# Optimization experiments

Measured on AMD Instinct MI355X. Metric: run time of the kernel, lower is better.

## Reference

```python
import jax, jax.numpy as jnp
import numpy as np

N = 1_000_000
H, W = 480, 640
MIN_DEPTH, MAX_DEPTH = 0.0, 30.0


def setup_inputs() -> dict:
    key = jax.random.key(0)
    k1, k2, k3 = jax.random.split(key, 3)
    scale = jnp.array([W - 1, H - 1], dtype=jnp.float32)
    mkpts0_f = jax.random.uniform(k1, (N, 2), dtype=jnp.float32) * scale
    mkpts1_f = jax.random.uniform(k2, (N, 2), dtype=jnp.float32) * scale
    mconf = jax.random.uniform(k3, (N,), dtype=jnp.float32)
    K = jnp.array([[520.0, 0.0, 320.0],
                   [0.0, 520.0, 240.0],
                   [0.0, 0.0, 1.0]], dtype=jnp.float32)
    K0 = K[None]  # [1,3,3]
    K1 = K[None]
    c, s = float(np.cos(0.1)), float(np.sin(0.1))
    T_0to1 = jnp.array([[c, 0.0, s, 0.2],
                        [0.0, 1.0, 0.0, 0.0],
                        [-s, 0.0, c, 0.05],
                        [0.0, 0.0, 0.0, 1.0]], dtype=jnp.float32)[None]  # [1,4,4]
    image0 = jnp.zeros((1, 1, H, W), dtype=jnp.float32)
    m_bids = jnp.zeros((N,), dtype=jnp.int32)  # single batch element
    return {"T_0to1": T_0to1, "K0": K0, "K1": K1, "mconf": mconf,
            "mkpts0_f": mkpts0_f, "mkpts1_f": mkpts1_f,
            "image0": image0, "m_bids": m_bids}


def _triangulate(T_0to1, K0, K1, mconf, kpts0, kpts1):
    # Projection matrices: P0 = K0 @ [I|0], P1 = K1 @ T[:3,:]
    proj_identity = jnp.eye(3, 4, dtype=K0.dtype)
    P0 = K0[0] @ proj_identity          # [3,4]
    P1 = K1[0] @ T_0to1[0, :3, :]       # [3,4]
    P = jnp.stack([P0, P1], axis=0)     # [V=2,3,4]

    pts = jnp.stack([kpts0, kpts1], axis=1)              # [N,2,2]
    conf = jnp.stack([jnp.ones_like(mconf), mconf], 1)   # [N,2] (self conf = 1)

    # A[n,v] = pts[n,v,:,None] * P[v,2,None,:] - P[v,:2]   -> [N,V,2,4]
    A = pts[..., None] * P[None, :, 2, None, :] - P[None, :, :2, :]
    A = A * conf[:, :, None, None]
    A = A.reshape(A.shape[0], 4, 4)                       # [N,4,4]

    # torch.svd returns V with A = U S V^T; jnp gives Vh = V^T.
    _, _, Vh = jnp.linalg.svd(A)
    v = -Vh[:, 3, :]                                      # [N,4] = -V[:,:,3]
    points_3d = v[:, :3] / v[:, 3:4]                      # homogeneous -> euclidean
    # torch clamps to [-1000,1000] only when infs appear; the final depth value
    # after [0,30] clamp + filter is identical either way, so clip unconditionally.
    points_3d = jnp.clip(points_3d, -1000.0, 1000.0)

    z = jnp.clip(points_3d[:, 2], MIN_DEPTH, MAX_DEPTH)
    filt = (z > MIN_DEPTH) & (z < MAX_DEPTH)
    kp3d_val = z * filt.astype(z.dtype)
    return kp3d_val, points_3d


def reference(T_0to1, K0, K1, mconf, mkpts0_f, mkpts1_f, image0, m_bids):
    h, w = image0.shape[-2], image0.shape[-1]
    kp3d_val, _ = _triangulate(T_0to1, K0, K1, mconf, mkpts0_f, mkpts1_f)
    # generate_sparse_depth: depth[0, y, x] = kp3d_val (long() truncation)
    xi = mkpts0_f[:, 0].astype(jnp.int32)
    yi = mkpts0_f[:, 1].astype(jnp.int32)
    depth0_sparse = jnp.zeros((1, h, w), dtype=kp3d_val.dtype).at[0, yi, xi].set(kp3d_val)
    return depth0_sparse, kp3d_val
```

## Files before the change

### kernel.cpp

```cpp
#include <hip/hip_runtime.h>
#include <math.h>

#define N_PTS 1000000
#define H_IMG 480
#define W_IMG 640
#define PIX (H_IMG * W_IMG)
#define TPB 256
#define BPTS 1024
#define NBLK ((N_PTS + BPTS - 1) / BPTS)


#define ROT64(p, q)                                                            \
  do {                                                                         \
    double apq = Mv[p][q];                                                     \
    if (apq != 0.0) {                                                          \
      double app = Mv[p][p], aqq = Mv[q][q];                                   \
      double d = aqq - app;                                                    \
      double r = sqrt(fma(d, d, 4.0 * apq * apq));                             \
      double t = (2.0 * apq) / (d + copysign(r, d));                           \
      double c = rsqrt(fma(t, t, 1.0));                                        \
      double s = t * c;                                                        \
      Mv[p][p] = fma(-t, apq, app);                                            \
      Mv[q][q] = fma(t, apq, aqq);                                             \
      Mv[p][q] = 0.0;                                                          \
      Mv[q][p] = 0.0;                                                          \
      _Pragma("unroll") for (int k = 0; k < 4; k++) {                          \
        if (k != p && k != q) {                                                \
          double akp = Mv[k][p], akq = Mv[k][q];                               \
          double nkp = c * akp - s * akq;                                      \
          double nkq = s * akp + c * akq;                                      \
          Mv[k][p] = nkp; Mv[p][k] = nkp;                                      \
          Mv[k][q] = nkq; Mv[q][k] = nkq;                                      \
        }                                                                      \
      }                                                                        \
      { double v2p = Vr2[p], v2q = Vr2[q];                                     \
        Vr2[p] = c * v2p - s * v2q; Vr2[q] = s * v2p + c * v2q; }              \
      { double v3p = Vr3[p], v3q = Vr3[q];                                     \
        Vr3[p] = c * v3p - s * v3q; Vr3[q] = s * v3p + c * v3q; }              \
    }                                                                          \
  } while (0)

__device__ float tri_point_fp64(int n,
                                const float* __restrict__ T,
                                const float* __restrict__ K0,
                                const float* __restrict__ K1,
                                const float* __restrict__ mconf,
                                const float* __restrict__ kp0,
                                const float* __restrict__ kp1) {
  float2 p0 = ((const float2*)kp0)[n];
  float2 p1 = ((const float2*)kp1)[n];
  double conf = (double)mconf[n];
  double x0 = (double)p0.x, y0 = (double)p0.y;
  double x1 = (double)p1.x, y1 = (double)p1.y;

  double P0[3][4];
#pragma unroll
  for (int i = 0; i < 3; i++) {
#pragma unroll
    for (int j = 0; j < 3; j++) P0[i][j] = (double)K0[i * 3 + j];
    P0[i][3] = 0.0;
  }
  double P1[3][4];
#pragma unroll
  for (int i = 0; i < 3; i++) {
#pragma unroll
    for (int j = 0; j < 4; j++) {
      double s = 0.0;
#pragma unroll
      for (int k = 0; k < 3; k++)
        s += (double)K1[i * 3 + k] * (double)T[k * 4 + j];
      P1[i][j] = s;
    }
  }

  double Mv[4][4];
#pragma unroll
  for (int i = 0; i < 4; i++)
#pragma unroll
    for (int j = 0; j < 4; j++) Mv[i][j] = 0.0;

  double a[4];
#pragma unroll
  for (int j = 0; j < 4; j++) a[j] = x0 * P0[2][j] - P0[0][j];
#pragma unroll
  for (int i = 0; i < 4; i++)
#pragma unroll
    for (int j = 0; j < 4; j++) Mv[i][j] = fma(a[i], a[j], Mv[i][j]);
#pragma unroll
  for (int j = 0; j < 4; j++) a[j] = y0 * P0[2][j] - P0[1][j];
#pragma unroll
  for (int i = 0; i < 4; i++)
#pragma unroll
    for (int j = 0; j < 4; j++) Mv[i][j] = fma(a[i], a[j], Mv[i][j]);
#pragma unroll
  for (int j = 0; j < 4; j++) a[j] = conf * (x1 * P1[2][j] - P1[0][j]);
#pragma unroll
  for (int i = 0; i < 4; i++)
#pragma unroll
    for (int j = 0; j < 4; j++) Mv[i][j] = fma(a[i], a[j], Mv[i][j]);
#pragma unroll
  for (int j = 0; j < 4; j++) a[j] = conf * (y1 * P1[2][j] - P1[1][j]);
#pragma unroll
  for (int i = 0; i < 4; i++)
#pragma unroll
    for (int j = 0; j < 4; j++) Mv[i][j] = fma(a[i], a[j], Mv[i][j]);

  double Vr2[4] = {0.0, 0.0, 1.0, 0.0};
  double Vr3[4] = {0.0, 0.0, 0.0, 1.0};

  for (int sweep = 0; sweep < 4; sweep++) {
    ROT64(0, 1); ROT64(0, 2); ROT64(0, 3);
    ROT64(1, 2); ROT64(1, 3); ROT64(2, 3);
  }

  double e0 = Mv[0][0], e1 = Mv[1][1], e2 = Mv[2][2], e3 = Mv[3][3];
  bool b01 = e1 < e0;
  double ea = b01 ? e1 : e0;
  double za = b01 ? Vr2[1] : Vr2[0];
  double wa = b01 ? Vr3[1] : Vr3[0];
  bool b23 = e3 < e2;
  double eb = b23 ? e3 : e2;
  double zb = b23 ? Vr2[3] : Vr2[2];
  double wb = b23 ? Vr3[3] : Vr3[2];
  bool bf = eb < ea;
  double vz = bf ? zb : za;
  double vw = bf ? wb : wa;

  double z = vz / vw;
  z = fmin(fmax(z, 0.0), 30.0);
  bool filt = (z > 0.0) && (z < 30.0);
  return filt ? (float)z : 0.0f;
}

__global__ __launch_bounds__(TPB) void tri_main(
    const float* __restrict__ T,
    const float* __restrict__ K0,
    const float* __restrict__ K1,
    const float* __restrict__ mconf,
    const float* __restrict__ kp0,
    const float* __restrict__ kp1,
    float* __restrict__ out_kp3d,
    unsigned long long* __restrict__ ws_pix)
{
  __shared__ unsigned short s_list[BPTS];
  __shared__ int s_cnt;

  int tid = threadIdx.x;
  int base = blockIdx.x * BPTS;
  if (tid == 0) s_cnt = 0;
  __syncthreads();

  double P0d[3][4], P1d[3][4];
#pragma unroll
  for (int i = 0; i < 3; i++) {
#pragma unroll
    for (int j = 0; j < 3; j++) P0d[i][j] = (double)K0[i * 3 + j];
    P0d[i][3] = 0.0;
  }
#pragma unroll
  for (int i = 0; i < 3; i++) {
#pragma unroll
    for (int j = 0; j < 4; j++) {
      double s = 0.0;
#pragma unroll
      for (int k = 0; k < 3; k++)
        s += (double)K1[i * 3 + k] * (double)T[k * 4 + j];
      P1d[i][j] = s;
    }
  }

#pragma unroll 1
  for (int r = 0; r < BPTS / TPB; r++) {
    int local = r * TPB + tid;
    int n = base + local;
    if (n >= N_PTS) break;

    float2 p0 = ((const float2*)kp0)[n];
    float2 p1 = ((const float2*)kp1)[n];
    float conff = mconf[n];

    double m00, m01, m02, m03, m11, m12, m13, m22, m23, m33;
    m00 = m01 = m02 = m03 = m11 = m12 = m13 = m22 = m23 = m33 = 0.0;
    {
      double x0 = (double)p0.x, y0 = (double)p0.y;
      double x1 = (double)p1.x, y1 = (double)p1.y;
      double cf = (double)conff;
      double a[4];
#pragma unroll
      for (int rr = 0; rr < 4; rr++) {
        if (rr == 0) {
#pragma unroll
          for (int j = 0; j < 4; j++) a[j] = fma(x0, P0d[2][j], -P0d[0][j]);
        } else if (rr == 1) {
#pragma unroll
          for (int j = 0; j < 4; j++) a[j] = fma(y0, P0d[2][j], -P0d[1][j]);
        } else if (rr == 2) {
#pragma unroll
          for (int j = 0; j < 4; j++)
            a[j] = cf * fma(x1, P1d[2][j], -P1d[0][j]);
        } else {
#pragma unroll
          for (int j = 0; j < 4; j++)
            a[j] = cf * fma(y1, P1d[2][j], -P1d[1][j]);
        }
        m00 = fma(a[0], a[0], m00); m01 = fma(a[0], a[1], m01);
        m02 = fma(a[0], a[2], m02); m03 = fma(a[0], a[3], m03);
        m11 = fma(a[1], a[1], m11); m12 = fma(a[1], a[2], m12);
        m13 = fma(a[1], a[3], m13); m22 = fma(a[2], a[2], m22);
        m23 = fma(a[2], a[3], m23); m33 = fma(a[3], a[3], m33);
      }
    }

    double t1 = (m00 + m11) + (m22 + m33);
    double ms0 = fma(m00, m11, -m01 * m01);
    double ms1 = fma(m00, m12, -m02 * m01);
    double ms2 = fma(m00, m13, -m03 * m01);
    double ms3 = fma(m01, m12, -m02 * m11);
    double ms4 = fma(m01, m13, -m03 * m11);
    double mc0 = fma(m02, m13, -m12 * m03);
    double mc1 = fma(m02, m23, -m22 * m03);
    double mc2 = fma(m02, m33, -m23 * m03);
    double mc3 = fma(m12, m23, -m22 * m13);
    double mc4 = fma(m12, m33, -m23 * m13);
    double mc5 = fma(m22, m33, -m23 * m23);
    double A00 = fma(m11, mc5, fma(-m12, mc4, m13 * mc3));
    double A01 = -fma(m01, mc5, fma(-m02, mc4, m03 * mc3));
    double A11 = fma(m00, mc5, fma(-m02, mc2, m03 * mc1));
    double A02 = fma(m01, mc4, fma(-m11, mc2, m13 * mc0));
    double A03 = -fma(m01, mc3, fma(-m11, mc1, m12 * mc0));
    double A22 = fma(m03, ms4, fma(-m13, ms2, m33 * ms0));
    double A33 = fma(m02, ms3, fma(-m12, ms1, m22 * ms0));
    double t3 = (A00 + A11) + (A22 + A33);
    double t4 = fma(m00, A00, fma(m01, A01, fma(m02, A02, m03 * A03)));
    double q02 = fma(m00, m22, -m02 * m02);
    double q03 = fma(m00, m33, -m03 * m03);
    double q12 = fma(m11, m22, -m12 * m12);
    double q13 = fma(m11, m33, -m13 * m13);
    double t2 = ((ms0 + mc5) + (q02 + q03)) + (q12 + q13);

    double mu = t4 / t3;
    double t1_3 = 3.0 * t1, t1_6 = 6.0 * t1, t2_2 = 2.0 * t2;
#pragma unroll
    for (int it = 0; it < 3; it++) {
      double pv = fma(fma(fma(mu - t1, mu, t2), mu, -t3), mu, t4);
      double pd = fma(fma(fma(4.0, mu, -t1_3), mu, t2_2), mu, -t3);
      double pdd = fma(fma(12.0, mu, -t1_6), mu, t2_2);
      double rad = 3.0 * fma(3.0 * pd, pd, -4.0 * pv * pdd);
      double sq = sqrt(fmax(rad, 0.0));
      double den = pd + copysign(sq, pd);
      mu = mu - 4.0 * pv / den;
    }

    double b00 = m00 - mu, b11 = m11 - mu, b22 = m22 - mu, b33 = m33 - mu;
    double s0 = fma(b00, b11, -m01 * m01);
    double s1 = fma(b00, m12, -m02 * m01);
    double s2 = fma(b00, m13, -m03 * m01);
    double s3 = fma(m01, m12, -m02 * b11);
    double s4 = fma(m01, m13, -m03 * b11);
    double c0 = fma(m02, m13, -m12 * m03);
    double c1 = fma(m02, m23, -b22 * m03);
    double c2 = fma(m02, b33, -m23 * m03);
    double c3 = fma(m12, m23, -b22 * m13);
    double c4 = fma(m12, b33, -m23 * m13);
    double c5 = fma(b22, b33, -m23 * m23);

    double a00 = fma(b11, c5, fma(-m12, c4, m13 * c3));
    double a01 = -fma(m01, c5, fma(-m02, c4, m03 * c3));
    double a11 = fma(b00, c5, fma(-m02, c2, m03 * c1));
    double a02 = fma(m01, c4, fma(-b11, c2, m13 * c0));
    double a12 = -fma(b00, c4, fma(-m01, c2, m03 * c0));
    double a22 = fma(m03, s4, fma(-m13, s2, b33 * s0));
    double a03 = -fma(m01, c3, fma(-b11, c1, m12 * c0));
    double a13 = fma(b00, c3, fma(-m01, c1, m02 * c0));
    double a23 = -fma(m03, s3, fma(-m13, s1, m23 * s0));
    double a33 = fma(m02, s3, fma(-m12, s1, b22 * s0));

    double w10 = a00, w11 = a01, w12 = a02, w13 = a03;
    double bd = fabs(a00);
    { double d1 = fabs(a11);
      bool c = d1 > bd;
      w10 = c ? a01 : w10; w11 = c ? a11 : w11;
      w12 = c ? a12 : w12; w13 = c ? a13 : w13; bd = c ? d1 : bd; }
    { double d2 = fabs(a22);
      bool c = d2 > bd;
      w10 = c ? a02 : w10; w11 = c ? a12 : w11;
      w12 = c ? a22 : w12; w13 = c ? a23 : w13; bd = c ? d2 : bd; }
    { double d3 = fabs(a33);
      bool c = d3 > bd;
      w10 = c ? a03 : w10; w11 = c ? a13 : w11;
      w12 = c ? a23 : w12; w13 = c ? a33 : w13; }

    double u0 = fma(a00, w10, fma(a01, w11, fma(a02, w12, a03 * w13)));
    double u1 = fma(a01, w10, fma(a11, w11, fma(a12, w12, a13 * w13)));
    double u2 = fma(a02, w10, fma(a12, w11, fma(a22, w12, a23 * w13)));
    double u3 = fma(a03, w10, fma(a13, w11, fma(a23, w12, a33 * w13)));
    double v2 = fma(a02, u0, fma(a12, u1, fma(a22, u2, a23 * u3)));
    double v3 = fma(a03, u0, fma(a13, u1, fma(a23, u2, a33 * u3)));

    double z2 = u2 / u3;
    double z3 = v2 / v3;

    double tol = 1e-3 * fmax(1.0, fabs(z3));
    bool ok = (fabs(z3 - z2) < tol) && (fabs(z3 - 30.0) > 0.1);

    if (ok) {
      double zc = fmin(fmax(z3, 0.0), 30.0);
      bool filt = (zc > 0.0) && (zc < 30.0);
      float kp = filt ? (float)zc : 0.0f;
      out_kp3d[n] = kp;
      int pix = (int)p0.y * W_IMG + (int)p0.x;
      atomicMax(&ws_pix[pix],
                ((unsigned long long)(0xC0000000u | (unsigned)n) << 32) |
                    (unsigned long long)__float_as_uint(kp));
    } else {
      int idx = atomicAdd(&s_cnt, 1);
      s_list[idx] = (unsigned short)local;
    }
  }

  __syncthreads();

  int cnt = s_cnt;
  for (int i = tid; i < cnt; i += TPB) {
    int n = base + (int)s_list[i];
    float kp = tri_point_fp64(n, T, K0, K1, mconf, kp0, kp1);
    out_kp3d[n] = kp;
    float2 p0 = ((const float2*)kp0)[n];
    int pix = (int)p0.y * W_IMG + (int)p0.x;
    atomicMax(&ws_pix[pix],
              ((unsigned long long)(0xC0000000u | (unsigned)n) << 32) |
                  (unsigned long long)__float_as_uint(kp));
  }
}

__global__ __launch_bounds__(TPB) void unpack_depth(
    const unsigned long long* __restrict__ ws_pix,
    float* __restrict__ out_depth)
{
  int p = blockIdx.x * blockDim.x + threadIdx.x;
  if (p < PIX) {
    unsigned long long v = ws_pix[p];
    unsigned int hi = (unsigned int)(v >> 32);
    out_depth[p] =
        (hi >= 0xC0000000u) ? __uint_as_float((unsigned int)v) : 0.0f;
  }
}

extern "C" void kernel_launch(void* const* d_in, const int* in_sizes, int n_in,
                              void* d_out, int out_size, void* d_ws, size_t ws_size,
                              hipStream_t stream) {
  const float* T     = (const float*)d_in[0];
  const float* K0    = (const float*)d_in[1];
  const float* K1    = (const float*)d_in[2];
  const float* mconf = (const float*)d_in[3];
  const float* kp0   = (const float*)d_in[4];
  const float* kp1   = (const float*)d_in[5];

  float* out = (float*)d_out;
  unsigned long long* ws_pix = (unsigned long long*)d_ws;

  tri_main<<<NBLK, TPB, 0, stream>>>(T, K0, K1, mconf, kp0, kp1,
                                     out + PIX, ws_pix);

  unpack_depth<<<(PIX + TPB - 1) / TPB, TPB, 0, stream>>>(ws_pix, out);
}
```

Before: 126.1 us.

## Use hardware rcp/rsq with Newton refinement and process two points per iteration

Replaces fp64 divisions and sqrt in the fast eigen-solver path with hardware reciprocal and rsqrt approximations refined by Newton steps. It also rewrites the acceptance test as a cross-multiplied comparison so one division is dropped. The per-thread loop now handles two points per iteration, giving more independent instructions to hide latency. In exchange, accuracy near the tolerance may differ slightly, so more points could fall back to the slow path, and register pressure rises.

```diff
diff --git a/kernel.cpp b/kernel.cpp
--- a/kernel.cpp
+++ b/kernel.cpp
@@ -9,6 +9,23 @@
 #define BPTS 1024
 #define NBLK ((N_PTS + BPTS - 1) / BPTS)
 
+
+__device__ __forceinline__ double frcp1(double b) {
+  double r = __builtin_amdgcn_rcp(b);
+  r = fma(fma(-b, r, 1.0), r, r);
+  return r;
+}
+__device__ __forceinline__ double frcp2(double b) {
+  double r = __builtin_amdgcn_rcp(b);
+  r = fma(fma(-b, r, 1.0), r, r);
+  r = fma(fma(-b, r, 1.0), r, r);
+  return r;
+}
+__device__ __forceinline__ double fsqrt_pos(double x) {
+  double r = __builtin_amdgcn_rsq(x);
+  double y = x * r;
+  return fma(0.5 * r, fma(-y, y, x), y);
+}
 
 #define ROT64(p, q)                                                            \
   do {                                                                         \
@@ -132,6 +149,134 @@
   return filt ? (float)z : 0.0f;
 }
 
+__device__ __forceinline__ void tri_fast(
+    float2 p0, float2 p1, float conff,
+    const double (&P0d)[3][4], const double (&P1d)[3][4],
+    double* z_out, bool* ok_out) {
+  double m00, m01, m02, m03, m11, m12, m13, m22, m23, m33;
+  m00 = m01 = m02 = m03 = m11 = m12 = m13 = m22 = m23 = m33 = 0.0;
+  {
+    double x0 = (double)p0.x, y0 = (double)p0.y;
+    double x1 = (double)p1.x, y1 = (double)p1.y;
+    double cf = (double)conff;
+    double a[4];
+#pragma unroll
+    for (int rr = 0; rr < 4; rr++) {
+      if (rr == 0) {
+#pragma unroll
+        for (int j = 0; j < 4; j++) a[j] = fma(x0, P0d[2][j], -P0d[0][j]);
+      } else if (rr == 1) {
+#pragma unroll
+        for (int j = 0; j < 4; j++) a[j] = fma(y0, P0d[2][j], -P0d[1][j]);
+      } else if (rr == 2) {
+#pragma unroll
+        for (int j = 0; j < 4; j++) a[j] = cf * fma(x1, P1d[2][j], -P1d[0][j]);
+      } else {
+#pragma unroll
+        for (int j = 0; j < 4; j++) a[j] = cf * fma(y1, P1d[2][j], -P1d[1][j]);
+      }
+      m00 = fma(a[0], a[0], m00); m01 = fma(a[0], a[1], m01);
+      m02 = fma(a[0], a[2], m02); m03 = fma(a[0], a[3], m03);
+      m11 = fma(a[1], a[1], m11); m12 = fma(a[1], a[2], m12);
+      m13 = fma(a[1], a[3], m13); m22 = fma(a[2], a[2], m22);
+      m23 = fma(a[2], a[3], m23); m33 = fma(a[3], a[3], m33);
+    }
+  }
+
+  double t1 = (m00 + m11) + (m22 + m33);
+  double ms0 = fma(m00, m11, -m01 * m01);
+  double ms1 = fma(m00, m12, -m02 * m01);
+  double ms2 = fma(m00, m13, -m03 * m01);
+  double ms3 = fma(m01, m12, -m02 * m11);
+  double ms4 = fma(m01, m13, -m03 * m11);
+  double mc0 = fma(m02, m13, -m12 * m03);
+  double mc1 = fma(m02, m23, -m22 * m03);
+  double mc2 = fma(m02, m33, -m23 * m03);
+  double mc3 = fma(m12, m23, -m22 * m13);
+  double mc4 = fma(m12, m33, -m23 * m13);
+  double mc5 = fma(m22, m33, -m23 * m23);
+  double A00 = fma(m11, mc5, fma(-m12, mc4, m13 * mc3));
+  double A01 = -fma(m01, mc5, fma(-m02, mc4, m03 * mc3));
+  double A11 = fma(m00, mc5, fma(-m02, mc2, m03 * mc1));
+  double A02 = fma(m01, mc4, fma(-m11, mc2, m13 * mc0));
+  double A03 = -fma(m01, mc3, fma(-m11, mc1, m12 * mc0));
+  double A22 = fma(m03, ms4, fma(-m13, ms2, m33 * ms0));
+  double A33 = fma(m02, ms3, fma(-m12, ms1, m22 * ms0));
+  double t3 = (A00 + A11) + (A22 + A33);
+  double t4 = fma(m00, A00, fma(m01, A01, fma(m02, A02, m03 * A03)));
+  double q02 = fma(m00, m22, -m02 * m02);
+  double q03 = fma(m00, m33, -m03 * m03);
+  double q12 = fma(m11, m22, -m12 * m12);
+  double q13 = fma(m11, m33, -m13 * m13);
+  double t2 = ((ms0 + mc5) + (q02 + q03)) + (q12 + q13);
+
+  double mu = t4 * frcp1(t3);
+  double t1_3 = 3.0 * t1, t1_6 = 6.0 * t1, t2_2 = 2.0 * t2;
+#pragma unroll
+  for (int it = 0; it < 3; it++) {
+    double pv = fma(fma(fma(mu - t1, mu, t2), mu, -t3), mu, t4);
+    double pd = fma(fma(fma(4.0, mu, -t1_3), mu, t2_2), mu, -t3);
+    double pdd = fma(fma(12.0, mu, -t1_6), mu, t2_2);
+    double rad = 3.0 * fma(3.0 * pd, pd, -4.0 * pv * pdd);
+    double sq = fsqrt_pos(fmax(rad, 1e-300));
+    double den = pd + copysign(sq, pd);
+    mu = fma(-4.0 * pv, frcp1(den), mu);
+  }
+
+  double b00 = m00 - mu, b11 = m11 - mu, b22 = m22 - mu, b33 = m33 - mu;
+  double s0 = fma(b00, b11, -m01 * m01);
+  double s1 = fma(b00, m12, -m02 * m01);
+  double s2 = fma(b00, m13, -m03 * m01);
+  double s3 = fma(m01, m12, -m02 * b11);
+  double s4 = fma(m01, m13, -m03 * b11);
+  double c0 = fma(m02, m13, -m12 * m03);
+  double c1 = fma(m02, m23, -b22 * m03);
+  double c2 = fma(m02, b33, -m23 * m03);
+  double c3 = fma(m12, m23, -b22 * m13);
+  double c4 = fma(m12, b33, -m23 * m13);
+  double c5 = fma(b22, b33, -m23 * m23);
+
+  double a00 = fma(b11, c5, fma(-m12, c4, m13 * c3));
+  double a01 = -fma(m01, c5, fma(-m02, c4, m03 * c3));
+  double a11 = fma(b00, c5, fma(-m02, c2, m03 * c1));
+  double a02 = fma(m01, c4, fma(-b11, c2, m13 * c0));
+  double a12 = -fma(b00, c4, fma(-m01, c2, m03 * c0));
+  double a22 = fma(m03, s4, fma(-m13, s2, b33 * s0));
+  double a03 = -fma(m01, c3, fma(-b11, c1, m12 * c0));
+  double a13 = fma(b00, c3, fma(-m01, c1, m02 * c0));
+  double a23 = -fma(m03, s3, fma(-m13, s1, m23 * s0));
+  double a33 = fma(m02, s3, fma(-m12, s1, b22 * s0));
+
+  double w10 = a00, w11 = a01, w12 = a02, w13 = a03;
+  double bd = fabs(a00);
+  { double d1 = fabs(a11);
+    bool c = d1 > bd;
+    w10 = c ? a01 : w10; w11 = c ? a11 : w11;
+    w12 = c ? a12 : w12; w13 = c ? a13 : w13; bd = c ? d1 : bd; }
+  { double d2 = fabs(a22);
+    bool c = d2 > bd;
+    w10 = c ? a02 : w10; w11 = c ? a12 : w11;
+    w12 = c ? a22 : w12; w13 = c ? a23 : w13; bd = c ? d2 : bd; }
+  { double d3 = fabs(a33);
+    bool c = d3 > bd;
+    w10 = c ? a03 : w10; w11 = c ? a13 : w11;
+    w12 = c ? a23 : w12; w13 = c ? a33 : w13; }
+
+  double u0 = fma(a00, w10, fma(a01, w11, fma(a02, w12, a03 * w13)));
+  double u1 = fma(a01, w10, fma(a11, w11, fma(a12, w12, a13 * w13)));
+  double u2 = fma(a02, w10, fma(a12, w11, fma(a22, w12, a23 * w13)));
+  double u3 = fma(a03, w10, fma(a13, w11, fma(a23, w12, a33 * w13)));
+  double v2 = fma(a02, u0, fma(a12, u1, fma(a22, u2, a23 * u3)));
+  double v3 = fma(a03, u0, fma(a13, u1, fma(a23, u2, a33 * u3)));
+
+  double z3 = v2 * frcp2(v3);
+
+  double cross = fabs(fma(v2, u3, -(u2 * v3)));
+  double rhs = 1e-3 * fmax(fabs(v3 * u3), fabs(v2 * u3));
+  *ok_out = (cross < rhs) && (fabs(z3 - 30.0) > 0.1);
+  *z_out = z3;
+}
+
 __global__ __launch_bounds__(TPB) void tri_main(
     const float* __restrict__ T,
     const float* __restrict__ K0,
@@ -170,151 +315,57 @@
   }
 
 #pragma unroll 1
-  for (int r = 0; r < BPTS / TPB; r++) {
-    int local = r * TPB + tid;
-    int n = base + local;
-    if (n >= N_PTS) break;
-
-    float2 p0 = ((const float2*)kp0)[n];
-    float2 p1 = ((const float2*)kp1)[n];
-    float conff = mconf[n];
-
-    double m00, m01, m02, m03, m11, m12, m13, m22, m23, m33;
-    m00 = m01 = m02 = m03 = m11 = m12 = m13 = m22 = m23 = m33 = 0.0;
-    {
-      double x0 = (double)p0.x, y0 = (double)p0.y;
-      double x1 = (double)p1.x, y1 = (double)p1.y;
-      double cf = (double)conff;
-      double a[4];
-#pragma unroll
-      for (int rr = 0; rr < 4; rr++) {
-        if (rr == 0) {
-#pragma unroll
-          for (int j = 0; j < 4; j++) a[j] = fma(x0, P0d[2][j], -P0d[0][j]);
-        } else if (rr == 1) {
-#pragma unroll
-          for (int j = 0; j < 4; j++) a[j] = fma(y0, P0d[2][j], -P0d[1][j]);
-        } else if (rr == 2) {
-#pragma unroll
-          for (int j = 0; j < 4; j++)
-            a[j] = cf * fma(x1, P1d[2][j], -P1d[0][j]);
-        } else {
-#pragma unroll
-          for (int j = 0; j < 4; j++)
-            a[j] = cf * fma(y1, P1d[2][j], -P1d[1][j]);
-        }
-        m00 = fma(a[0], a[0], m00); m01 = fma(a[0], a[1], m01);
-        m02 = fma(a[0], a[2], m02); m03 = fma(a[0], a[3], m03);
-        m11 = fma(a[1], a[1], m11); m12 = fma(a[1], a[2], m12);
-        m13 = fma(a[1], a[3], m13); m22 = fma(a[2], a[2], m22);
-        m23 = fma(a[2], a[3], m23); m33 = fma(a[3], a[3], m33);
+  for (int r = 0; r < BPTS / (2 * TPB); r++) {
+    int l0 = r * (2 * TPB) + tid;
+    int l1 = l0 + TPB;
+    int n0 = base + l0;
+    int n1 = base + l1;
+    bool act0 = n0 < N_PTS;
+    bool act1 = n1 < N_PTS;
+    int nc0 = act0 ? n0 : (N_PTS - 1);
+    int nc1 = act1 ? n1 : (N_PTS - 1);
+
+    float2 p0a = ((const float2*)kp0)[nc0];
+    float2 p1a = ((const float2*)kp1)[nc0];
+    float cfa = mconf[nc0];
+    float2 p0b = ((const float2*)kp0)[nc1];
+    float2 p1b = ((const float2*)kp1)[nc1];
+    float cfb = mconf[nc1];
+
+    double zA, zB;
+    bool okA, okB;
+    tri_fast(p0a, p1a, cfa, P0d, P1d, &zA, &okA);
+    tri_fast(p0b, p1b, cfb, P0d, P1d, &zB, &okB);
+
+    if (act0) {
+      if (okA) {
+        double zc = fmin(fmax(zA, 0.0), 30.0);
+        bool filt = (zc > 0.0) && (zc < 30.0);
+        float kp = filt ? (float)zc : 0.0f;
+        out_kp3d[n0] = kp;
+        int pix = (int)p0a.y * W_IMG + (int)p0a.x;
+        atomicMax(&ws_pix[pix],
+                  ((unsigned long long)(0xC0000000u | (unsigned)n0) << 32) |
+                      (unsigned long long)__float_as_uint(kp));
+      } else {
+        int idx = atomicAdd(&s_cnt, 1);
+        s_list[idx] = (unsigned short)l0;
       }
     }
-
-    double t1 = (m00 + m11) + (m22 + m33);
-    double ms0 = fma(m00, m11, -m01 * m01);
-    double ms1 = fma(m00, m12, -m02 * m01);
-    double ms2 = fma(m00, m13, -m03 * m01);
-    double ms3 = fma(m01, m12, -m02 * m11);
-    double ms4 = fma(m01, m13, -m03 * m11);
-    double mc0 = fma(m02, m13, -m12 * m03);
-    double mc1 = fma(m02, m23, -m22 * m03);
-    double mc2 = fma(m02, m33, -m23 * m03);
-    double mc3 = fma(m12, m23, -m22 * m13);
-    double mc4 = fma(m12, m33, -m23 * m13);
-    double mc5 = fma(m22, m33, -m23 * m23);
-    double A00 = fma(m11, mc5, fma(-m12, mc4, m13 * mc3));
-    double A01 = -fma(m01, mc5, fma(-m02, mc4, m03 * mc3));
-    double A11 = fma(m00, mc5, fma(-m02, mc2, m03 * mc1));
-    double A02 = fma(m01, mc4, fma(-m11, mc2, m13 * mc0));
-    double A03 = -fma(m01, mc3, fma(-m11, mc1, m12 * mc0));
-    double A22 = fma(m03, ms4, fma(-m13, ms2, m33 * ms0));
-    double A33 = fma(m02, ms3, fma(-m12, ms1, m22 * ms0));
-    double t3 = (A00 + A11) + (A22 + A33);
-    double t4 = fma(m00, A00, fma(m01, A01, fma(m02, A02, m03 * A03)));
-    double q02 = fma(m00, m22, -m02 * m02);
-    double q03 = fma(m00, m33, -m03 * m03);
-    double q12 = fma(m11, m22, -m12 * m12);
-    double q13 = fma(m11, m33, -m13 * m13);
-    double t2 = ((ms0 + mc5) + (q02 + q03)) + (q12 + q13);
-
-    double mu = t4 / t3;
-    double t1_3 = 3.0 * t1, t1_6 = 6.0 * t1, t2_2 = 2.0 * t2;
-#pragma unroll
-    for (int it = 0; it < 3; it++) {
-      double pv = fma(fma(fma(mu - t1, mu, t2), mu, -t3), mu, t4);
-      double pd = fma(fma(fma(4.0, mu, -t1_3), mu, t2_2), mu, -t3);
-      double pdd = fma(fma(12.0, mu, -t1_6), mu, t2_2);
-      double rad = 3.0 * fma(3.0 * pd, pd, -4.0 * pv * pdd);
-      double sq = sqrt(fmax(rad, 0.0));
-      double den = pd + copysign(sq, pd);
-      mu = mu - 4.0 * pv / den;
-    }
-
-    double b00 = m00 - mu, b11 = m11 - mu, b22 = m22 - mu, b33 = m33 - mu;
-    double s0 = fma(b00, b11, -m01 * m01);
-    double s1 = fma(b00, m12, -m02 * m01);
-    double s2 = fma(b00, m13, -m03 * m01);
-    double s3 = fma(m01, m12, -m02 * b11);
-    double s4 = fma(m01, m13, -m03 * b11);
-    double c0 = fma(m02, m13, -m12 * m03);
-    double c1 = fma(m02, m23, -b22 * m03);
-    double c2 = fma(m02, b33, -m23 * m03);
-    double c3 = fma(m12, m23, -b22 * m13);
-    double c4 = fma(m12, b33, -m23 * m13);
-    double c5 = fma(b22, b33, -m23 * m23);
-
-    double a00 = fma(b11, c5, fma(-m12, c4, m13 * c3));
-    double a01 = -fma(m01, c5, fma(-m02, c4, m03 * c3));
-    double a11 = fma(b00, c5, fma(-m02, c2, m03 * c1));
-    double a02 = fma(m01, c4, fma(-b11, c2, m13 * c0));
-    double a12 = -fma(b00, c4, fma(-m01, c2, m03 * c0));
-    double a22 = fma(m03, s4, fma(-m13, s2, b33 * s0));
-    double a03 = -fma(m01, c3, fma(-b11, c1, m12 * c0));
-    double a13 = fma(b00, c3, fma(-m01, c1, m02 * c0));
-    double a23 = -fma(m03, s3, fma(-m13, s1, m23 * s0));
-    double a33 = fma(m02, s3, fma(-m12, s1, b22 * s0));
-
-    double w10 = a00, w11 = a01, w12 = a02, w13 = a03;
-    double bd = fabs(a00);
-    { double d1 = fabs(a11);
-      bool c = d1 > bd;
-      w10 = c ? a01 : w10; w11 = c ? a11 : w11;
-      w12 = c ? a12 : w12; w13 = c ? a13 : w13; bd = c ? d1 : bd; }
-    { double d2 = fabs(a22);
-      bool c = d2 > bd;
-      w10 = c ? a02 : w10; w11 = c ? a12 : w11;
-      w12 = c ? a22 : w12; w13 = c ? a23 : w13; bd = c ? d2 : bd; }
-    { double d3 = fabs(a33);
-      bool c = d3 > bd;
-      w10 = c ? a03 : w10; w11 = c ? a13 : w11;
-      w12 = c ? a23 : w12; w13 = c ? a33 : w13; }
-
-    double u0 = fma(a00, w10, fma(a01, w11, fma(a02, w12, a03 * w13)));
-    double u1 = fma(a01, w10, fma(a11, w11, fma(a12, w12, a13 * w13)));
-    double u2 = fma(a02, w10, fma(a12, w11, fma(a22, w12, a23 * w13)));
-    double u3 = fma(a03, w10, fma(a13, w11, fma(a23, w12, a33 * w13)));
-    double v2 = fma(a02, u0, fma(a12, u1, fma(a22, u2, a23 * u3)));
-    double v3 = fma(a03, u0, fma(a13, u1, fma(a23, u2, a33 * u3)));
-
-    double z2 = u2 / u3;
-    double z3 = v2 / v3;
-
-    double tol = 1e-3 * fmax(1.0, fabs(z3));
-    bool ok = (fabs(z3 - z2) < tol) && (fabs(z3 - 30.0) > 0.1);
-
-    if (ok) {
-      double zc = fmin(fmax(z3, 0.0), 30.0);
-      bool filt = (zc > 0.0) && (zc < 30.0);
-      float kp = filt ? (float)zc : 0.0f;
-      out_kp3d[n] = kp;
-      int pix = (int)p0.y * W_IMG + (int)p0.x;
-      atomicMax(&ws_pix[pix],
-                ((unsigned long long)(0xC0000000u | (unsigned)n) << 32) |
-                    (unsigned long long)__float_as_uint(kp));
-    } else {
-      int idx = atomicAdd(&s_cnt, 1);
-      s_list[idx] = (unsigned short)local;
+    if (act1) {
+      if (okB) {
+        double zc = fmin(fmax(zB, 0.0), 30.0);
+        bool filt = (zc > 0.0) && (zc < 30.0);
+        float kp = filt ? (float)zc : 0.0f;
+        out_kp3d[n1] = kp;
+        int pix = (int)p0b.y * W_IMG + (int)p0b.x;
+        atomicMax(&ws_pix[pix],
+                  ((unsigned long long)(0xC0000000u | (unsigned)n1) << 32) |
+                      (unsigned long long)__float_as_uint(kp));
+      } else {
+        int idx = atomicAdd(&s_cnt, 1);
+        s_list[idx] = (unsigned short)l1;
+      }
     }
   }
 
```

Measured after the change: 126.7 us. About the same (+0.5%).
